# Performance work log

Hardware: AMD Instinct MI355X
Metric: run time of the kernel (lower is better)

The kernel has to match this reference:

```python
import jax, jax.numpy as jnp
import numpy as np

# (multiplicity, irrep dimension 2l+1) for irreps_in == irreps_out == 128x0e+128x1o+128x2e
IRREPS = [(128, 1), (128, 3), (128, 5)]
N_NODES = 100000
DIM = sum(m * d for m, d in IRREPS)  # 1152
W_NUMEL = sum(m * m for m, _ in IRREPS)  # 49152
B_NUMEL = IRREPS[0][0]  # bias only on scalar 0e irrep -> 128


def setup_inputs() -> dict:
    key = jax.random.key(0)
    k1, k2, k3 = jax.random.split(key, 3)
    x = jax.random.normal(k1, (N_NODES, DIM), dtype=jnp.float32)
    w = jax.random.normal(k2, (W_NUMEL,), dtype=jnp.float32)
    b = jax.random.normal(k3, (B_NUMEL,), dtype=jnp.float32)
    return {"x": x, "w": w, "b": b}


def reference(x, w, b):
    # Segmented tensor-product linear: one small (mul_in x mul_out) matmul per irrep
    # segment, scaled by path_weight = (sum of contributing mul_in)^-0.5 = 128^-0.5,
    # then bias (path_weight 1.0) added only on the scalar 0e output slice.
    outs = []
    off_x = 0
    off_w = 0
    for idx, (mul, d) in enumerate(IRREPS):
        seg = x[:, off_x:off_x + mul * d].reshape(-1, mul, d)  # [N, mul, 2l+1]
        W = w[off_w:off_w + mul * mul].reshape(mul, mul)       # [mul_in, mul_out]
        pw = 1.0 / np.sqrt(mul)                                # element normalization
        o = pw * jnp.einsum('nui,uv->nvi', seg, W)             # [N, mul, 2l+1]
        if idx == 0:
            o = o + b.reshape(mul, d)                          # bias on scalars only
        outs.append(o.reshape(-1, mul * d))
        off_x += mul * d
        off_w += mul * mul
    return jnp.concatenate(outs, axis=-1)  # [N, DIM]
```

## Files before the change

### kernel.cpp

```cpp
#include <hip/hip_runtime.h>

typedef __attribute__((ext_vector_type(8))) short bf16x8;
typedef __attribute__((ext_vector_type(4))) float f32x4;

#define NBLK   16
#define DIMF   1152
#define NTILE  6250
#define GRIDSZ 512
#define ROWU   1160

static __device__ __forceinline__ unsigned short f2bf(float f) {
    unsigned int u = __builtin_bit_cast(unsigned int, f);
    return (unsigned short)((u + 0x7FFFu + ((u >> 16) & 1u)) >> 16);
}

__global__ __launch_bounds__(512, 2)
void seglin_kernel(const float* __restrict__ x, const float* __restrict__ w,
                   const float* __restrict__ b, float* __restrict__ out) {
    __shared__ unsigned short xs[2][NBLK][ROWU];

    const int tid  = threadIdx.x;
    const int wv   = tid >> 6;
    const int lane = tid & 63;
    const int lq   = lane & 15;
    const int lg   = lane >> 4;
    const int v0   = wv * 16;

    const int sn = tid >> 5;
    const int st = tid & 31;

    const float pw = 0.08838834764831845f;

    bf16x8 wf[3][4];
    const int woff[3] = {0, 16384, 32768};
    #pragma unroll
    for (int s = 0; s < 3; ++s)
        #pragma unroll
        for (int t = 0; t < 4; ++t) {
            bf16x8 f;
            #pragma unroll
            for (int e = 0; e < 8; ++e) {
                int u = 32 * t + lg * 8 + e;
                f[e] = (short)f2bf(pw * w[woff[s] + u * 128 + v0 + lq]);
            }
            wf[s][t] = f;
        }

    float biasr[4];
    #pragma unroll
    for (int e = 0; e < 4; ++e) biasr[e] = b[v0 + lg * 4 + e];

    float4 g0, g1[3], g2[5];

#define STAGE_LOAD(TILE) do {                                                   \
        const float* src = x + ((long)(TILE) * NBLK + sn) * DIMF;               \
        g0    = *reinterpret_cast<const float4*>(src + 4 * st);                 \
        g1[0] = *reinterpret_cast<const float4*>(src + 128 + 12 * st);          \
        g1[1] = *reinterpret_cast<const float4*>(src + 128 + 12 * st + 4);      \
        g1[2] = *reinterpret_cast<const float4*>(src + 128 + 12 * st + 8);      \
        g2[0] = *reinterpret_cast<const float4*>(src + 512 + 20 * st);          \
        g2[1] = *reinterpret_cast<const float4*>(src + 512 + 20 * st + 4);      \
        g2[2] = *reinterpret_cast<const float4*>(src + 512 + 20 * st + 8);      \
        g2[3] = *reinterpret_cast<const float4*>(src + 512 + 20 * st + 12);     \
        g2[4] = *reinterpret_cast<const float4*>(src + 512 + 20 * st + 16);     \
    } while (0)

#define STAGE_WRITE(BUF) do {                                                   \
        unsigned short* dst = &xs[BUF][sn][0];                                  \
        { ushort4 h;                                                            \
          h.x = f2bf(g0.x); h.y = f2bf(g0.y); h.z = f2bf(g0.z); h.w = f2bf(g0.w); \
          *reinterpret_cast<ushort4*>(dst + 4 * st) = h; }                      \
        float f1[12], f2[20];                                                   \
        f1[0]=g1[0].x; f1[1]=g1[0].y; f1[2]=g1[0].z; f1[3]=g1[0].w;             \
        f1[4]=g1[1].x; f1[5]=g1[1].y; f1[6]=g1[1].z; f1[7]=g1[1].w;             \
        f1[8]=g1[2].x; f1[9]=g1[2].y; f1[10]=g1[2].z; f1[11]=g1[2].w;           \
        _Pragma("unroll")                                                       \
        for (int i = 0; i < 3; ++i) {                                           \
            ushort4 h;                                                          \
            h.x = f2bf(f1[0 + i]); h.y = f2bf(f1[3 + i]);                       \
            h.z = f2bf(f1[6 + i]); h.w = f2bf(f1[9 + i]);                       \
            *reinterpret_cast<ushort4*>(dst + 128 + (i << 7) + 4 * st) = h;     \
        }                                                                       \
        f2[0]=g2[0].x; f2[1]=g2[0].y; f2[2]=g2[0].z; f2[3]=g2[0].w;             \
        f2[4]=g2[1].x; f2[5]=g2[1].y; f2[6]=g2[1].z; f2[7]=g2[1].w;             \
        f2[8]=g2[2].x; f2[9]=g2[2].y; f2[10]=g2[2].z; f2[11]=g2[2].w;           \
        f2[12]=g2[3].x; f2[13]=g2[3].y; f2[14]=g2[3].z; f2[15]=g2[3].w;         \
        f2[16]=g2[4].x; f2[17]=g2[4].y; f2[18]=g2[4].z; f2[19]=g2[4].w;         \
        _Pragma("unroll")                                                       \
        for (int i = 0; i < 5; ++i) {                                           \
            ushort4 h;                                                          \
            h.x = f2bf(f2[0 + i]);  h.y = f2bf(f2[5 + i]);                      \
            h.z = f2bf(f2[10 + i]); h.w = f2bf(f2[15 + i]);                     \
            *reinterpret_cast<ushort4*>(dst + 512 + (i << 7) + 4 * st) = h;     \
        }                                                                       \
    } while (0)

    long tile = blockIdx.x;
    STAGE_LOAD(tile);
    STAGE_WRITE(0);
    __syncthreads();

    int cur = 0;
    for (; tile < NTILE; tile += GRIDSZ) {
        f32x4 acc[9];
        #pragma unroll
        for (int q = 0; q < 9; ++q) {
            f32x4 z = {0.f, 0.f, 0.f, 0.f};
            acc[q] = z;
        }

        const unsigned short* row = &xs[cur][lq][0];
        #pragma unroll
        for (int t = 0; t < 4; ++t) {
            const int u0 = 32 * t + lg * 8;
            #pragma unroll
            for (int q = 0; q < 9; ++q) {
                const int s = (q == 0) ? 0 : (q < 4 ? 1 : 2);
                bf16x8 bf = *reinterpret_cast<const bf16x8*>(row + (q << 7) + u0);
                acc[q] = __builtin_amdgcn_mfma_f32_16x16x32_bf16(wf[s][t], bf, acc[q], 0, 0, 0);
            }
        }

        {
            float* orow = out + (tile * NBLK + lq) * (long)DIMF;
            const int vb = v0 + lg * 4;
            float4 o0;
            o0.x = acc[0][0] + biasr[0];
            o0.y = acc[0][1] + biasr[1];
            o0.z = acc[0][2] + biasr[2];
            o0.w = acc[0][3] + biasr[3];
            *reinterpret_cast<float4*>(orow + vb) = o0;
            float* p1o = orow + 128 + 3 * vb;
            #pragma unroll
            for (int k = 0; k < 3; ++k) {
                float4 o;
                o.x = acc[1 + ((4 * k + 0) % 3)][(4 * k + 0) / 3];
                o.y = acc[1 + ((4 * k + 1) % 3)][(4 * k + 1) / 3];
                o.z = acc[1 + ((4 * k + 2) % 3)][(4 * k + 2) / 3];
                o.w = acc[1 + ((4 * k + 3) % 3)][(4 * k + 3) / 3];
                *reinterpret_cast<float4*>(p1o + 4 * k) = o;
            }
            float* p2o = orow + 512 + 5 * vb;
            #pragma unroll
            for (int k = 0; k < 5; ++k) {
                float4 o;
                o.x = acc[4 + ((4 * k + 0) % 5)][(4 * k + 0) / 5];
                o.y = acc[4 + ((4 * k + 1) % 5)][(4 * k + 1) / 5];
                o.z = acc[4 + ((4 * k + 2) % 5)][(4 * k + 2) / 5];
                o.w = acc[4 + ((4 * k + 3) % 5)][(4 * k + 3) / 5];
                *reinterpret_cast<float4*>(p2o + 4 * k) = o;
            }
        }

        if (tile + GRIDSZ < NTILE) {
            STAGE_LOAD(tile + GRIDSZ);
            STAGE_WRITE(cur ^ 1);
        }

        asm volatile("s_waitcnt lgkmcnt(0)\n\ts_barrier" ::: "memory");
        cur ^= 1;
    }
#undef STAGE_LOAD
#undef STAGE_WRITE
}

extern "C" void kernel_launch(void* const* d_in, const int* in_sizes, int n_in,
                              void* d_out, int out_size, void* d_ws, size_t ws_size,
                              hipStream_t stream) {
    const float* x = (const float*)d_in[0];
    const float* w = (const float*)d_in[1];
    const float* b = (const float*)d_in[2];
    float* outp = (float*)d_out;
    seglin_kernel<<<dim3(GRIDSZ), dim3(512), 0, stream>>>(x, w, b, outp);
}
```

Before: 209.1 us.

## Issue next-tile global loads before MFMA and split compute per irrep segment

The global loads for the next tile now start at the top of the loop iteration, before the MFMA compute and output stores, instead of after them. This lets HBM read latency overlap with compute. The single 9-accumulator MFMA loop is split into three per-segment blocks (0e, 1o, 2e), each storing its output right after computing it. This lowers live accumulator registers and interleaves stores with compute, but the prefetched float4 registers (36 floats) stay live across the whole compute, which raises register pressure under launch_bounds(512,2).

```diff
diff --git a/kernel.cpp b/kernel.cpp
--- a/kernel.cpp
+++ b/kernel.cpp
@@ -102,60 +102,80 @@
 
     int cur = 0;
     for (; tile < NTILE; tile += GRIDSZ) {
-        f32x4 acc[9];
-        #pragma unroll
-        for (int q = 0; q < 9; ++q) {
-            f32x4 z = {0.f, 0.f, 0.f, 0.f};
-            acc[q] = z;
+        const bool has_next = (tile + GRIDSZ) < NTILE;
+
+        if (has_next) STAGE_LOAD(tile + GRIDSZ);
+
+        const unsigned short* row = &xs[cur][lq][0];
+        float* orow = out + (tile * NBLK + lq) * (long)DIMF;
+        const int vb = v0 + lg * 4;
+
+        {
+            f32x4 a0 = {0.f, 0.f, 0.f, 0.f};
+            #pragma unroll
+            for (int t = 0; t < 4; ++t) {
+                bf16x8 bf = *reinterpret_cast<const bf16x8*>(row + 32 * t + lg * 8);
+                a0 = __builtin_amdgcn_mfma_f32_16x16x32_bf16(wf[0][t], bf, a0, 0, 0, 0);
+            }
+            float4 o0;
+            o0.x = a0[0] + biasr[0];
+            o0.y = a0[1] + biasr[1];
+            o0.z = a0[2] + biasr[2];
+            o0.w = a0[3] + biasr[3];
+            *reinterpret_cast<float4*>(orow + vb) = o0;
         }
 
-        const unsigned short* row = &xs[cur][lq][0];
-        #pragma unroll
-        for (int t = 0; t < 4; ++t) {
-            const int u0 = 32 * t + lg * 8;
+        {
+            f32x4 aB[3];
             #pragma unroll
-            for (int q = 0; q < 9; ++q) {
-                const int s = (q == 0) ? 0 : (q < 4 ? 1 : 2);
-                bf16x8 bf = *reinterpret_cast<const bf16x8*>(row + (q << 7) + u0);
-                acc[q] = __builtin_amdgcn_mfma_f32_16x16x32_bf16(wf[s][t], bf, acc[q], 0, 0, 0);
+            for (int j = 0; j < 3; ++j) { f32x4 z = {0.f,0.f,0.f,0.f}; aB[j] = z; }
+            #pragma unroll
+            for (int t = 0; t < 4; ++t) {
+                const int u0 = 32 * t + lg * 8;
+                #pragma unroll
+                for (int j = 0; j < 3; ++j) {
+                    bf16x8 bf = *reinterpret_cast<const bf16x8*>(row + ((1 + j) << 7) + u0);
+                    aB[j] = __builtin_amdgcn_mfma_f32_16x16x32_bf16(wf[1][t], bf, aB[j], 0, 0, 0);
+                }
+            }
+            float* p1o = orow + 128 + 3 * vb;
+            #pragma unroll
+            for (int k = 0; k < 3; ++k) {
+                float4 o;
+                o.x = aB[(4 * k + 0) % 3][(4 * k + 0) / 3];
+                o.y = aB[(4 * k + 1) % 3][(4 * k + 1) / 3];
+                o.z = aB[(4 * k + 2) % 3][(4 * k + 2) / 3];
+                o.w = aB[(4 * k + 3) % 3][(4 * k + 3) / 3];
+                *reinterpret_cast<float4*>(p1o + 4 * k) = o;
             }
         }
 
         {
-            float* orow = out + (tile * NBLK + lq) * (long)DIMF;
-            const int vb = v0 + lg * 4;
-            float4 o0;
-            o0.x = acc[0][0] + biasr[0];
-            o0.y = acc[0][1] + biasr[1];
-            o0.z = acc[0][2] + biasr[2];
-            o0.w = acc[0][3] + biasr[3];
-            *reinterpret_cast<float4*>(orow + vb) = o0;
-            float* p1o = orow + 128 + 3 * vb;
+            f32x4 aC[5];
             #pragma unroll
-            for (int k = 0; k < 3; ++k) {
-                float4 o;
-                o.x = acc[1 + ((4 * k + 0) % 3)][(4 * k + 0) / 3];
-                o.y = acc[1 + ((4 * k + 1) % 3)][(4 * k + 1) / 3];
-                o.z = acc[1 + ((4 * k + 2) % 3)][(4 * k + 2) / 3];
-                o.w = acc[1 + ((4 * k + 3) % 3)][(4 * k + 3) / 3];
-                *reinterpret_cast<float4*>(p1o + 4 * k) = o;
+            for (int j = 0; j < 5; ++j) { f32x4 z = {0.f,0.f,0.f,0.f}; aC[j] = z; }
+            #pragma unroll
+            for (int t = 0; t < 4; ++t) {
+                const int u0 = 32 * t + lg * 8;
+                #pragma unroll
+                for (int j = 0; j < 5; ++j) {
+                    bf16x8 bf = *reinterpret_cast<const bf16x8*>(row + ((4 + j) << 7) + u0);
+                    aC[j] = __builtin_amdgcn_mfma_f32_16x16x32_bf16(wf[2][t], bf, aC[j], 0, 0, 0);
+                }
             }
             float* p2o = orow + 512 + 5 * vb;
             #pragma unroll
             for (int k = 0; k < 5; ++k) {
                 float4 o;
-                o.x = acc[4 + ((4 * k + 0) % 5)][(4 * k + 0) / 5];
-                o.y = acc[4 + ((4 * k + 1) % 5)][(4 * k + 1) / 5];
-                o.z = acc[4 + ((4 * k + 2) % 5)][(4 * k + 2) / 5];
-                o.w = acc[4 + ((4 * k + 3) % 5)][(4 * k + 3) / 5];
+                o.x = aC[(4 * k + 0) % 5][(4 * k + 0) / 5];
+                o.y = aC[(4 * k + 1) % 5][(4 * k + 1) / 5];
+                o.z = aC[(4 * k + 2) % 5][(4 * k + 2) / 5];
+                o.w = aC[(4 * k + 3) % 5][(4 * k + 3) / 5];
                 *reinterpret_cast<float4*>(p2o + 4 * k) = o;
             }
         }
 
-        if (tile + GRIDSZ < NTILE) {
-            STAGE_LOAD(tile + GRIDSZ);
-            STAGE_WRITE(cur ^ 1);
-        }
+        if (has_next) STAGE_WRITE(cur ^ 1);
 
         asm volatile("s_waitcnt lgkmcnt(0)\n\ts_barrier" ::: "memory");
         cur ^= 1;
```

Measured after the change: 187.4 us. 10.4% less time.
